# Kernel tuning notes

Hardware: AMD Instinct MI355X
Metric: run time of the kernel (lower is better)

Reference implementation:

```python
import jax, jax.numpy as jnp
import numpy as np

CHANNELS = 128
HEADS = 4
R = 2
LAMBDA = 0.1


def setup_inputs() -> dict:
    key = jax.random.key(0)
    k1, k2 = jax.random.split(key)
    x = jax.random.normal(k1, (1, CHANNELS, 32, 32, 32), dtype=jnp.float32)
    # 1x1x1 Conv3d weight [3C, C] (trailing unit spatial dims dropped), fan-in scaled
    w_qkv = jax.random.normal(k2, (3 * CHANNELS, CHANNELS), dtype=jnp.float32) * (CHANNELS ** -0.5)
    return {"x": x, "w_qkv": w_qkv}


def reference(x, w_qkv):
    head_dim = CHANNELS // HEADS          # 32
    d_half = head_dim // 2                # 16
    scale = head_dim ** -0.5
    # AvgPool3d(kernel_size=1, stride=R) == strided subsampling
    xs = x[:, :, ::R, ::R, ::R]
    B, C, H, W, Z = xs.shape
    N = H * W * Z                          # 4096 tokens
    # 1x1x1 conv == pointwise channel matmul, then group channels heads-major
    qkv = jnp.einsum('oc,bchwz->bohwz', w_qkv, xs).reshape(B, HEADS, 3 * head_dim, N)
    q, k, v = jnp.split(qkv, 3, axis=2)    # each [B, h, head_dim, N]
    q1, q2 = q[:, :, :d_half, :], q[:, :, d_half:, :]
    k1, k2 = k[:, :, :d_half, :], k[:, :, d_half:, :]
    # two full score matrices [B, h, N, N] (differential attention)
    attn1 = jnp.einsum('bhdn,bhdm->bhnm', q1, k1) * scale
    attn2 = jnp.einsum('bhdn,bhdm->bhnm', q2, k2) * scale
    diff_attn = jax.nn.softmax(attn1, axis=-1) - LAMBDA * jax.nn.softmax(attn2, axis=-1)
    out = jnp.einsum('bhnm,bhdm->bhnd', diff_attn, v)  # [B, h, N, head_dim]
    # faithful to torch .view(B, -1, H, W, Z) on contiguous (h, N, head_dim) layout
    return out.reshape(B, C, H, W, Z)
```

## Files before the change

### kernel.cpp

```cpp
#include <hip/hip_runtime.h>

#define N_TOK 4096
#define NH    4

typedef __attribute__((ext_vector_type(8))) short bf16x8;
typedef __attribute__((ext_vector_type(4))) short bf16x4;
typedef __attribute__((ext_vector_type(4))) float f32x4;

static constexpr float SCALE   = 0.17677669529663687f;
static constexpr float QSCALE  = 0.25503632254435463f;
static constexpr float LAMBDA_ = 0.1f;
#define PSTRIDE 2112

__device__ __forceinline__ unsigned short bf_rne(float f) {
    unsigned u = __float_as_uint(f);
    u += 0x7FFF + ((u >> 16) & 1);
    return (unsigned short)(u >> 16);
}

__device__ __forceinline__ void async_copy16(const unsigned short* g, unsigned short* l) {
    __builtin_amdgcn_global_load_lds(
        (const __attribute__((address_space(1))) void*)g,
        (__attribute__((address_space(3))) void*)l, 16, 0, 0);
}

__global__ __launch_bounds__(256) void qkv_kernel(
    const float* __restrict__ x, const float* __restrict__ wsrc,
    unsigned short* __restrict__ qA, unsigned short* __restrict__ kB,
    unsigned short* __restrict__ vT)
{
    __shared__ __align__(16) float xf[16][132];
    __shared__ __align__(16) unsigned short xbh[16 * 136];
    __shared__ __align__(16) unsigned short xbl[16 * 136];
    __shared__ __align__(16) unsigned short qsh[2][16][64];
    __shared__ __align__(16) unsigned short ksh[2][16][64];
    __shared__ __align__(16) unsigned short vsh[2][32][16];

    const int t  = threadIdx.x;
    const int tg = blockIdx.x >> 1;
    const int rh = blockIdx.x & 1;
    const int n0 = tg * 16;
    const int nh = n0 >> 8, nw = (n0 >> 4) & 15;
    const int xbase = nh * 2048 + nw * 64;

    #pragma unroll
    for (int k = 0; k < 4; ++k) {
        int idx = t + k * 256;
        int pair = idx & 7, ch = idx >> 3;
        float4 f4 = *(const float4*)&x[(size_t)ch * 32768 + xbase + pair * 4];
        xf[pair * 2][ch]     = f4.x;
        xf[pair * 2 + 1][ch] = f4.z;
    }
    __syncthreads();
    #pragma unroll
    for (int k = 0; k < 8; ++k) {
        int idx = t + k * 256;
        int tok = idx & 15, ch = idx >> 4;
        float f = xf[tok][ch];
        unsigned u = __float_as_uint(f);
        float lo = f - __uint_as_float(u & 0xFFFF0000u);
        xbh[tok * 136 + ch] = (unsigned short)(u >> 16);
        xbl[tok * 136 + ch] = (unsigned short)(__float_as_uint(lo) >> 16);
    }
    __syncthreads();

    const int lane = t & 63;
    const int m    = lane & 15;
    const int quad = lane >> 4;
    const int w    = t >> 6;

    bf16x8 Bh[4], Bl[4];
    #pragma unroll
    for (int s = 0; s < 4; ++s) {
        Bh[s] = *(const bf16x8*)&xbh[m * 136 + s * 32 + quad * 8];
        Bl[s] = *(const bf16x8*)&xbl[m * 136 + s * 32 + quad * 8];
    }

    #pragma unroll
    for (int rt = 0; rt < 3; ++rt) {
        const int R0 = rh * 192 + w * 48 + rt * 16;
        const int row = R0 + m;
        const int rr_row = row % 96;
        const float sc = (rr_row < 32) ? QSCALE : 1.0f;
        const float* wp = wsrc + (size_t)row * 128;
        bf16x8 Ah[4], Al[4];
        #pragma unroll
        for (int s = 0; s < 4; ++s) {
            float4 f0 = *(const float4*)(wp + s * 32 + quad * 8);
            float4 f1 = *(const float4*)(wp + s * 32 + quad * 8 + 4);
            float fv[8] = {f0.x, f0.y, f0.z, f0.w, f1.x, f1.y, f1.z, f1.w};
            #pragma unroll
            for (int j = 0; j < 8; ++j) {
                float f = fv[j] * sc;
                unsigned u = __float_as_uint(f);
                float lo = f - __uint_as_float(u & 0xFFFF0000u);
                Ah[s][j] = (short)(unsigned short)(u >> 16);
                Al[s][j] = (short)(unsigned short)(__float_as_uint(lo) >> 16);
            }
        }
        f32x4 C = {0, 0, 0, 0};
        #pragma unroll
        for (int s = 0; s < 4; ++s) {
            C = __builtin_amdgcn_mfma_f32_16x16x32_bf16(Ah[s], Bh[s], C, 0, 0, 0);
            C = __builtin_amdgcn_mfma_f32_16x16x32_bf16(Al[s], Bh[s], C, 0, 0, 0);
            C = __builtin_amdgcn_mfma_f32_16x16x32_bf16(Ah[s], Bl[s], C, 0, 0, 0);
        }
        #pragma unroll
        for (int i = 0; i < 4; ++i) {
            int R  = R0 + quad * 4 + i;
            int hh = R / 96;
            int rr = R - hh * 96;
            int hl = hh & 1;
            float f = C[i];
            if (rr < 64) {
                unsigned u = __float_as_uint(f);
                float lo = f - __uint_as_float(u & 0xFFFF0000u);
                unsigned short hi16 = (unsigned short)(u >> 16);
                unsigned short lo16 = (unsigned short)(__float_as_uint(lo) >> 16);
                int part = (rr & 31) >> 4, d = rr & 15;
                if (rr < 32) {
                    qsh[hl][m][part * 32 + d]      = hi16;
                    qsh[hl][m][part * 32 + d + 16] = lo16;
                } else {
                    ksh[hl][m][part * 32 + d]      = hi16;
                    ksh[hl][m][part * 32 + d + 16] = lo16;
                }
            } else {
                vsh[hl][rr - 64][m] = bf_rne(f);
            }
        }
    }
    __syncthreads();

    {
        int rec = t >> 3, ch8 = t & 7;
        int hl  = rec >> 4, i = rec & 15;
        int hh  = rh * 2 + hl;
        size_t base = ((size_t)hh * N_TOK + n0 + i) * 64 + ch8 * 8;
        *(uint4*)(qA + base) = *(const uint4*)&qsh[hl][i][ch8 * 8];
        *(uint4*)(kB + base) = *(const uint4*)&ksh[hl][i][ch8 * 8];
    }
    if (t < 128) {
        int hl = t >> 6, d = (t >> 1) & 31, half = t & 1;
        int hh = rh * 2 + hl;
        int kb = (n0 >> 3) + half;
        *(uint4*)(vT + (size_t)hh * 131072 + kb * 256 + d * 8) =
            *(const uint4*)&vsh[hl][d][half * 8];
    }
}

__global__ __launch_bounds__(256, 4) void flash_kernel(
    const unsigned short* __restrict__ qA, const unsigned short* __restrict__ kB,
    const unsigned short* __restrict__ vT, float* __restrict__ parts)
{
    __shared__ __align__(16) unsigned short kv_sh[2][6144];
    __shared__ float Obuf[2][2][16][33];
    __shared__ float lbuf[2][2][16];

    const int t    = threadIdx.x;
    const int w    = t >> 6;
    const int lane = t & 63;
    const int m    = lane & 15;
    const int quad = lane >> 4;
    const int ks   = blockIdx.x & 1;
    const int qt   = (blockIdx.x >> 1) & 127;
    const int h    = blockIdx.x >> 8;
    const int qtile = w >> 1;
    const int kh    = w & 1;
    const int qbase = qt * 32;

    const unsigned short* kBh = kB + (size_t)h * N_TOK * 64;
    const unsigned short* vTh = vT + (size_t)h * 131072;
    const int key0 = ks * 2048;

    auto stage = [&](int tile, int b) {
        const unsigned short* kben = kBh + (size_t)(key0 + tile * 64) * 64;
        const unsigned short* vben = vTh + (size_t)((key0 >> 3) + tile * 8) * 256;
        #pragma unroll
        for (int i = 0; i < 3; ++i) {
            int s = i * 256 + t;
            const unsigned short* src;
            if (s < 512) {
                int ml = s >> 3, p = s & 7, c = p ^ (ml & 7);
                src = kben + ml * 64 + c * 8;
            } else {
                int s2 = s - 512;
                int kb_l = s2 >> 5, d = s2 & 31;
                src = vben + kb_l * 256 + d * 8;
            }
            async_copy16(src, &kv_sh[b][s * 8]);
        }
    };

    stage(0, 0);

    for (int i = t; i < 2112; i += 256) ((float*)Obuf)[i] = 0.f;
    if (t < 64) ((float*)lbuf)[t] = 0.f;

    const unsigned short* qrec = qA + (size_t)(h * N_TOK + qbase + qtile * 16 + m) * 64;
    const bf16x8 zz = {0,0,0,0,0,0,0,0};
    bf16x8 Bq1h = *(const bf16x8*)(qrec + (quad & 1) * 8);
    bf16x8 Bq2h = *(const bf16x8*)(qrec + 32 + (quad & 1) * 8);
    bf16x8 Bq1l = (quad < 2) ? *(const bf16x8*)(qrec + 16 + quad * 8) : zz;
    bf16x8 Bq2l = (quad < 2) ? *(const bf16x8*)(qrec + 48 + quad * 8) : zz;

    f32x4 O1a = {0,0,0,0}, O1b = {0,0,0,0}, O2a = {0,0,0,0}, O2b = {0,0,0,0};
    float l1 = 0.f, l2 = 0.f;

    const int ml0 = kh * 32 + m, ml1 = ml0 + 16;
    const int a1o0 = ml0 * 64 + ((quad)     ^ (ml0 & 7)) * 8;
    const int a2o0 = ml0 * 64 + ((4 + quad) ^ (ml0 & 7)) * 8;
    const int a1o1 = ml1 * 64 + ((quad)     ^ (ml1 & 7)) * 8;
    const int a2o1 = ml1 * 64 + ((4 + quad) ^ (ml1 & 7)) * 8;
    const int kbl0 = kh * 4 + (quad >> 1);
    const int v0o0 = 4096 + (kbl0 * 32 + m)      * 8 + (quad & 1) * 4;
    const int v1o0 = 4096 + (kbl0 * 32 + 16 + m) * 8 + (quad & 1) * 4;
    const int v0o1 = v0o0 + 512;
    const int v1o1 = v1o0 + 512;

    for (int tile = 0; tile < 32; ++tile) {
        const int b = tile & 1;
        __syncthreads();
        if (tile + 1 < 32) stage(tile + 1, b ^ 1);

        const unsigned short* buf = kv_sh[b];
        __builtin_amdgcn_s_setprio(1);
        bf16x8 K1_0 = *(const bf16x8*)(buf + a1o0);
        bf16x8 K2_0 = *(const bf16x8*)(buf + a2o0);
        bf16x8 K1_1 = *(const bf16x8*)(buf + a1o1);
        bf16x8 K2_1 = *(const bf16x8*)(buf + a2o1);

        f32x4 sA1 = {0,0,0,0}, sA2 = {0,0,0,0};
        f32x4 sB1 = {0,0,0,0}, sB2 = {0,0,0,0};
        sA1 = __builtin_amdgcn_mfma_f32_16x16x32_bf16(K1_0, Bq1h, sA1, 0, 0, 0);
        sB1 = __builtin_amdgcn_mfma_f32_16x16x32_bf16(K1_1, Bq1h, sB1, 0, 0, 0);
        sA1 = __builtin_amdgcn_mfma_f32_16x16x32_bf16(K1_0, Bq1l, sA1, 0, 0, 0);
        sB1 = __builtin_amdgcn_mfma_f32_16x16x32_bf16(K1_1, Bq1l, sB1, 0, 0, 0);
        sA2 = __builtin_amdgcn_mfma_f32_16x16x32_bf16(K2_0, Bq2h, sA2, 0, 0, 0);
        sB2 = __builtin_amdgcn_mfma_f32_16x16x32_bf16(K2_1, Bq2h, sB2, 0, 0, 0);
        sA2 = __builtin_amdgcn_mfma_f32_16x16x32_bf16(K2_0, Bq2l, sA2, 0, 0, 0);
        sB2 = __builtin_amdgcn_mfma_f32_16x16x32_bf16(K2_1, Bq2l, sB2, 0, 0, 0);

        float pa0 = __builtin_amdgcn_exp2f(sA1[0]), pa1 = __builtin_amdgcn_exp2f(sA1[1]);
        float pa2 = __builtin_amdgcn_exp2f(sA1[2]), pa3 = __builtin_amdgcn_exp2f(sA1[3]);
        float pb0 = __builtin_amdgcn_exp2f(sB1[0]), pb1 = __builtin_amdgcn_exp2f(sB1[1]);
        float pb2 = __builtin_amdgcn_exp2f(sB1[2]), pb3 = __builtin_amdgcn_exp2f(sB1[3]);
        float qa0 = __builtin_amdgcn_exp2f(sA2[0]), qa1 = __builtin_amdgcn_exp2f(sA2[1]);
        float qa2 = __builtin_amdgcn_exp2f(sA2[2]), qa3 = __builtin_amdgcn_exp2f(sA2[3]);
        float qb0 = __builtin_amdgcn_exp2f(sB2[0]), qb1 = __builtin_amdgcn_exp2f(sB2[1]);
        float qb2 = __builtin_amdgcn_exp2f(sB2[2]), qb3 = __builtin_amdgcn_exp2f(sB2[3]);
        l1 += (pa0 + pa1) + (pa2 + pa3) + (pb0 + pb1) + (pb2 + pb3);
        l2 += (qa0 + qa1) + (qa2 + qa3) + (qb0 + qb1) + (qb2 + qb3);
        union { unsigned u[2]; bf16x4 v; } cA1, cB1, cA2, cB2;
        cA1.u[0] = __builtin_amdgcn_perm(__float_as_uint(pa1), __float_as_uint(pa0), 0x07060302u);
        cA1.u[1] = __builtin_amdgcn_perm(__float_as_uint(pa3), __float_as_uint(pa2), 0x07060302u);
        cB1.u[0] = __builtin_amdgcn_perm(__float_as_uint(pb1), __float_as_uint(pb0), 0x07060302u);
        cB1.u[1] = __builtin_amdgcn_perm(__float_as_uint(pb3), __float_as_uint(pb2), 0x07060302u);
        cA2.u[0] = __builtin_amdgcn_perm(__float_as_uint(qa1), __float_as_uint(qa0), 0x07060302u);
        cA2.u[1] = __builtin_amdgcn_perm(__float_as_uint(qa3), __float_as_uint(qa2), 0x07060302u);
        cB2.u[0] = __builtin_amdgcn_perm(__float_as_uint(qb1), __float_as_uint(qb0), 0x07060302u);
        cB2.u[1] = __builtin_amdgcn_perm(__float_as_uint(qb3), __float_as_uint(qb2), 0x07060302u);

        bf16x4 V00 = *(const bf16x4*)(buf + v0o0);
        bf16x4 V10 = *(const bf16x4*)(buf + v1o0);
        bf16x4 V01 = *(const bf16x4*)(buf + v0o1);
        bf16x4 V11 = *(const bf16x4*)(buf + v1o1);

        O1a = __builtin_amdgcn_mfma_f32_16x16x16bf16_1k(cA1.v, V00, O1a, 0, 0, 0);
        O1b = __builtin_amdgcn_mfma_f32_16x16x16bf16_1k(cA1.v, V10, O1b, 0, 0, 0);
        O2a = __builtin_amdgcn_mfma_f32_16x16x16bf16_1k(cA2.v, V00, O2a, 0, 0, 0);
        O2b = __builtin_amdgcn_mfma_f32_16x16x16bf16_1k(cA2.v, V10, O2b, 0, 0, 0);
        O1a = __builtin_amdgcn_mfma_f32_16x16x16bf16_1k(cB1.v, V01, O1a, 0, 0, 0);
        O1b = __builtin_amdgcn_mfma_f32_16x16x16bf16_1k(cB1.v, V11, O1b, 0, 0, 0);
        O2a = __builtin_amdgcn_mfma_f32_16x16x16bf16_1k(cB2.v, V01, O2a, 0, 0, 0);
        O2b = __builtin_amdgcn_mfma_f32_16x16x16bf16_1k(cB2.v, V11, O2b, 0, 0, 0);
        __builtin_amdgcn_s_setprio(0);
    }

    l1 += __shfl_xor(l1, 16, 64); l1 += __shfl_xor(l1, 32, 64);
    l2 += __shfl_xor(l2, 16, 64); l2 += __shfl_xor(l2, 32, 64);
    if (lane < 16) {
        atomicAdd(&lbuf[qtile][0][m], l1);
        atomicAdd(&lbuf[qtile][1][m], l2);
    }
    #pragma unroll
    for (int i = 0; i < 4; ++i) {
        int r = quad * 4 + i;
        atomicAdd(&Obuf[qtile][0][r][m],      O1a[i]);
        atomicAdd(&Obuf[qtile][0][r][16 + m], O1b[i]);
        atomicAdd(&Obuf[qtile][1][r][m],      O2a[i]);
        atomicAdd(&Obuf[qtile][1][r][16 + m], O2b[i]);
    }
    __syncthreads();

    float* dst = parts + (size_t)((h * 128 + qt) * 2 + ks) * PSTRIDE;
    for (int i = t; i < 1024; i += 256) {
        int r = i >> 5, d = i & 31;
        int qtl = r >> 4, rl = r & 15;
        dst[i]        = Obuf[qtl][0][rl][d];
        dst[1024 + i] = Obuf[qtl][1][rl][d];
    }
    if (t < 32) {
        int qtl = t >> 4, rl = t & 15;
        dst[2048 + t] = lbuf[qtl][0][rl];
        dst[2080 + t] = lbuf[qtl][1][rl];
    }
}

__global__ __launch_bounds__(256) void merge_kernel(
    const float* __restrict__ parts, float* __restrict__ out)
{
    int idx = blockIdx.x * 256 + threadIdx.x;
    int d4 = (idx & 7) * 4;
    int row = idx >> 3;
    int h = row >> 12, n = row & 4095;
    int qt = n >> 5, r = n & 31;
    const float* p0 = parts + (size_t)((h * 128 + qt) * 2) * PSTRIDE;
    const float* p1 = p0 + PSTRIDE;
    float4 a1 = *(const float4*)(p0 + r * 32 + d4);
    float4 b1 = *(const float4*)(p1 + r * 32 + d4);
    float4 a2 = *(const float4*)(p0 + 1024 + r * 32 + d4);
    float4 b2 = *(const float4*)(p1 + 1024 + r * 32 + d4);
    float l1 = p0[2048 + r] + p1[2048 + r];
    float l2 = p0[2080 + r] + p1[2080 + r];
    float4 o;
    o.x = (a1.x + b1.x) / l1 - LAMBDA_ * ((a2.x + b2.x) / l2);
    o.y = (a1.y + b1.y) / l1 - LAMBDA_ * ((a2.y + b2.y) / l2);
    o.z = (a1.z + b1.z) / l1 - LAMBDA_ * ((a2.z + b2.z) / l2);
    o.w = (a1.w + b1.w) / l1 - LAMBDA_ * ((a2.w + b2.w) / l2);
    *(float4*)(out + (size_t)idx * 4) = o;
}

extern "C" void kernel_launch(void* const* d_in, const int* in_sizes, int n_in,
                              void* d_out, int out_size, void* d_ws, size_t ws_size,
                              hipStream_t stream) {
    const float* x = (const float*)d_in[0];
    const float* w = (const float*)d_in[1];
    float* out = (float*)d_out;

    unsigned short* qA = (unsigned short*)d_ws;
    unsigned short* kB = qA + (size_t)NH * N_TOK * 64;
    unsigned short* vT = kB + (size_t)NH * N_TOK * 64;
    float* parts = (float*)(vT + (size_t)NH * 32 * N_TOK);

    qkv_kernel<<<512, 256, 0, stream>>>(x, w, qA, kB, vT);
    flash_kernel<<<1024, 256, 0, stream>>>(qA, kB, vT, parts);
    merge_kernel<<<512, 256, 0, stream>>>(parts, out);
}
```

Before: 133.0 us.

## Load K/V fragments directly from global memory instead of LDS double-buffer

Removes the async global-to-LDS double-buffered staging of K and V tiles and the per-tile __syncthreads. Each wave now reads its K and V fragments straight from global memory, relying on L1/L2 caching for the reuse between the two query-tile waves. This drops the block-wide barriers and the LDS footprint, which can raise occupancy. In exchange, global load latency is exposed in the inner loop with no explicit prefetch, and K/V data is fetched redundantly per wave.

```diff
diff --git a/kernel.cpp b/kernel.cpp
--- a/kernel.cpp
+++ b/kernel.cpp
@@ -16,12 +16,6 @@
     unsigned u = __float_as_uint(f);
     u += 0x7FFF + ((u >> 16) & 1);
     return (unsigned short)(u >> 16);
-}
-
-__device__ __forceinline__ void async_copy16(const unsigned short* g, unsigned short* l) {
-    __builtin_amdgcn_global_load_lds(
-        (const __attribute__((address_space(1))) void*)g,
-        (__attribute__((address_space(3))) void*)l, 16, 0, 0);
 }
 
 __global__ __launch_bounds__(256) void qkv_kernel(
@@ -153,7 +147,6 @@
     const unsigned short* __restrict__ qA, const unsigned short* __restrict__ kB,
     const unsigned short* __restrict__ vT, float* __restrict__ parts)
 {
-    __shared__ __align__(16) unsigned short kv_sh[2][6144];
     __shared__ float Obuf[2][2][16][33];
     __shared__ float lbuf[2][2][16];
 
@@ -173,29 +166,9 @@
     const unsigned short* vTh = vT + (size_t)h * 131072;
     const int key0 = ks * 2048;
 
-    auto stage = [&](int tile, int b) {
-        const unsigned short* kben = kBh + (size_t)(key0 + tile * 64) * 64;
-        const unsigned short* vben = vTh + (size_t)((key0 >> 3) + tile * 8) * 256;
-        #pragma unroll
-        for (int i = 0; i < 3; ++i) {
-            int s = i * 256 + t;
-            const unsigned short* src;
-            if (s < 512) {
-                int ml = s >> 3, p = s & 7, c = p ^ (ml & 7);
-                src = kben + ml * 64 + c * 8;
-            } else {
-                int s2 = s - 512;
-                int kb_l = s2 >> 5, d = s2 & 31;
-                src = vben + kb_l * 256 + d * 8;
-            }
-            async_copy16(src, &kv_sh[b][s * 8]);
-        }
-    };
-
-    stage(0, 0);
-
     for (int i = t; i < 2112; i += 256) ((float*)Obuf)[i] = 0.f;
     if (t < 64) ((float*)lbuf)[t] = 0.f;
+    __syncthreads();
 
     const unsigned short* qrec = qA + (size_t)(h * N_TOK + qbase + qtile * 16 + m) * 64;
     const bf16x8 zz = {0,0,0,0,0,0,0,0};
@@ -208,28 +181,30 @@
     float l1 = 0.f, l2 = 0.f;
 
     const int ml0 = kh * 32 + m, ml1 = ml0 + 16;
-    const int a1o0 = ml0 * 64 + ((quad)     ^ (ml0 & 7)) * 8;
-    const int a2o0 = ml0 * 64 + ((4 + quad) ^ (ml0 & 7)) * 8;
-    const int a1o1 = ml1 * 64 + ((quad)     ^ (ml1 & 7)) * 8;
-    const int a2o1 = ml1 * 64 + ((4 + quad) ^ (ml1 & 7)) * 8;
     const int kbl0 = kh * 4 + (quad >> 1);
-    const int v0o0 = 4096 + (kbl0 * 32 + m)      * 8 + (quad & 1) * 4;
-    const int v1o0 = 4096 + (kbl0 * 32 + 16 + m) * 8 + (quad & 1) * 4;
-    const int v0o1 = v0o0 + 512;
-    const int v1o1 = v1o0 + 512;
-
-    for (int tile = 0; tile < 32; ++tile) {
-        const int b = tile & 1;
-        __syncthreads();
-        if (tile + 1 < 32) stage(tile + 1, b ^ 1);
-
-        const unsigned short* buf = kv_sh[b];
+    const int ka10 = ml0 * 64 + quad * 8;
+    const int ka20 = ml0 * 64 + (4 + quad) * 8;
+    const int ka11 = ml1 * 64 + quad * 8;
+    const int ka21 = ml1 * 64 + (4 + quad) * 8;
+    const int vo00 = (kbl0 * 32 + m) * 8 + (quad & 1) * 4;
+    const int vo10 = (kbl0 * 32 + 16 + m) * 8 + (quad & 1) * 4;
+    const int vo01 = vo00 + 512;
+    const int vo11 = vo10 + 512;
+
+    const unsigned short* kt = kBh + (size_t)key0 * 64;
+    const unsigned short* vt = vTh + (size_t)(key0 >> 3) * 256;
+
+    for (int tile = 0; tile < 32; ++tile, kt += 4096, vt += 2048) {
+        bf16x8 K1_0 = *(const bf16x8*)(kt + ka10);
+        bf16x8 K2_0 = *(const bf16x8*)(kt + ka20);
+        bf16x8 K1_1 = *(const bf16x8*)(kt + ka11);
+        bf16x8 K2_1 = *(const bf16x8*)(kt + ka21);
+        bf16x4 V00 = *(const bf16x4*)(vt + vo00);
+        bf16x4 V10 = *(const bf16x4*)(vt + vo10);
+        bf16x4 V01 = *(const bf16x4*)(vt + vo01);
+        bf16x4 V11 = *(const bf16x4*)(vt + vo11);
+
         __builtin_amdgcn_s_setprio(1);
-        bf16x8 K1_0 = *(const bf16x8*)(buf + a1o0);
-        bf16x8 K2_0 = *(const bf16x8*)(buf + a2o0);
-        bf16x8 K1_1 = *(const bf16x8*)(buf + a1o1);
-        bf16x8 K2_1 = *(const bf16x8*)(buf + a2o1);
-
         f32x4 sA1 = {0,0,0,0}, sA2 = {0,0,0,0};
         f32x4 sB1 = {0,0,0,0}, sB2 = {0,0,0,0};
         sA1 = __builtin_amdgcn_mfma_f32_16x16x32_bf16(K1_0, Bq1h, sA1, 0, 0, 0);
@@ -260,11 +235,6 @@
         cA2.u[1] = __builtin_amdgcn_perm(__float_as_uint(qa3), __float_as_uint(qa2), 0x07060302u);
         cB2.u[0] = __builtin_amdgcn_perm(__float_as_uint(qb1), __float_as_uint(qb0), 0x07060302u);
         cB2.u[1] = __builtin_amdgcn_perm(__float_as_uint(qb3), __float_as_uint(qb2), 0x07060302u);
-
-        bf16x4 V00 = *(const bf16x4*)(buf + v0o0);
-        bf16x4 V10 = *(const bf16x4*)(buf + v1o0);
-        bf16x4 V01 = *(const bf16x4*)(buf + v0o1);
-        bf16x4 V11 = *(const bf16x4*)(buf + v1o1);
 
         O1a = __builtin_amdgcn_mfma_f32_16x16x16bf16_1k(cA1.v, V00, O1a, 0, 0, 0);
         O1b = __builtin_amdgcn_mfma_f32_16x16x16bf16_1k(cA1.v, V10, O1b, 0, 0, 0);
```

Result: slower. 155.9 us (+17.2%).
